# Kernel optimization log

Measured on AMD Instinct MI355X. Metric: run time of the kernel, lower is better.

The kernel has to match this reference:

```python
import jax, jax.numpy as jnp
import numpy as np

B, C, N = 8, 256, 4096

def setup_inputs() -> dict:
    key = jax.random.key(0)
    k1, k2, k3 = jax.random.split(key, 3)
    pts_feat = jax.random.normal(k1, (B, C, N), dtype=jnp.float32)
    # Conv1d(channels, channels, 1, bias=False) weight is [C_out, C_in, 1] -> store as [C_out, C_in]
    scale = 1.0 / np.sqrt(C)
    Wq = jax.random.uniform(k2, (C, C), dtype=jnp.float32, minval=-scale, maxval=scale)
    Wk = jax.random.uniform(k3, (C, C), dtype=jnp.float32, minval=-scale, maxval=scale)
    return {"pts_feat": pts_feat, "Wq": Wq, "Wk": Wk}

def reference(pts_feat, Wq, Wk):
    # 1x1 conv == channel-wise matmul. x_q: [B, N, C], x_k: [B, C, N]
    x_q = jnp.einsum('bcn,dc->bnd', pts_feat, Wq)
    x_k = jnp.einsum('bcn,dc->bdn', pts_feat, Wk)
    logits = jnp.einsum('bnc,bcm->bnm', x_q, x_k)          # [B, N, N]
    attn = jax.nn.softmax(logits, axis=-1)
    attn = attn / (1e-8 + attn.sum(axis=-1, keepdims=True))
    # torch.einsum('bnn,bnc->bnc', attn, feat) takes the DIAGONAL of attn
    # and scales each point's raw feature vector by it (no contraction).
    diag = jnp.diagonal(attn, axis1=1, axis2=2)            # [B, N]
    x_attn = pts_feat * diag[:, None, :]                   # [B, C, N]
    return x_attn
```

## Files before the change

kernel.cpp:

```cpp
#include <hip/hip_runtime.h>
#include <hip/hip_bf16.h>
#include <cstdint>

#define B_ 8
#define C_ 256
#define N_ 4096

typedef __bf16 bf16;
typedef __bf16 bf16x8 __attribute__((ext_vector_type(8)));
typedef float f32x4 __attribute__((ext_vector_type(4)));
typedef unsigned int u32;

__device__ __forceinline__ void async_ld16(const void* g, void* l) {
  __builtin_amdgcn_global_load_lds(
      (const __attribute__((address_space(1))) void*)g,
      (__attribute__((address_space(3))) void*)l, 16, 0, 0);
}

__device__ __forceinline__ float bh2f(unsigned short u) {
  union { u32 i; float f; } x; x.i = ((u32)u) << 16; return x.f;
}
__device__ __forceinline__ unsigned short f2bh(float f) {
  union { float f; u32 i; } x; x.f = f;
  u32 i = x.i + 0x7fffu + ((x.i >> 16) & 1u);
  return (unsigned short)(i >> 16);
}

__device__ __forceinline__ bool wave_sniff_fp32(const unsigned short* p) {
  int l = threadIdx.x & 63;
  unsigned short u = p[2 * l];
  int e = (u >> 7) & 0xff;
  unsigned long long m = __ballot(e >= 112 && e <= 142);
  return __popcll(m) < 32;
}

__global__ __launch_bounds__(256) void k_pre(const void* __restrict__ Wqv,
                                             const void* __restrict__ Wkv,
                                             const void* __restrict__ Fv,
                                             unsigned short* __restrict__ Mt,
                                             unsigned short* __restrict__ Ft) {
  __shared__ float wkcol[C_];
  __shared__ unsigned short tile[64 * 66];
  int bid = blockIdx.x;
  int t = threadIdx.x;
  if (bid < 256) {
    bool fq = wave_sniff_fp32((const unsigned short*)Wqv);
    bool fk = wave_sniff_fp32((const unsigned short*)Wkv);
    int d = bid, c = t;
    if (fk)
      wkcol[c] = ((const float*)Wkv)[c * C_ + d];
    else
      wkcol[c] = bh2f(((const unsigned short*)Wkv)[c * C_ + d]);
    __syncthreads();
    float acc = 0.f;
    if (fq) {
      for (int e0 = 0; e0 < C_; e0 += 16) {
        float wq[16];
#pragma unroll
        for (int j = 0; j < 16; ++j) wq[j] = ((const float*)Wqv)[(e0 + j) * C_ + c];
#pragma unroll
        for (int j = 0; j < 16; ++j) acc += wkcol[e0 + j] * wq[j];
      }
    } else {
      for (int e0 = 0; e0 < C_; e0 += 16) {
        float wq[16];
#pragma unroll
        for (int j = 0; j < 16; ++j) wq[j] = bh2f(((const unsigned short*)Wqv)[(e0 + j) * C_ + c]);
#pragma unroll
        for (int j = 0; j < 16; ++j) acc += wkcol[e0 + j] * wq[j];
      }
    }
    Mt[(size_t)d * C_ + c] = f2bh(acc * 1.44269504f);
    return;
  }
  bool f32 = wave_sniff_fp32((const unsigned short*)Fv);
  int id = bid - 256;
  int n0 = (id & 63) * 64, c0 = ((id >> 6) & 3) * 64, b = id >> 8;
#pragma unroll
  for (int p = 0; p < 2; ++p) {
    int c = (t >> 3) + 32 * p;
    int n = (t & 7) * 8;
    size_t off = (size_t)(b * C_ + c0 + c) * N_ + n0 + n;
    unsigned short vals[8];
    if (f32) {
      const float* src = (const float*)Fv + off;
      float4 v0 = *(const float4*)(src);
      float4 v1 = *(const float4*)(src + 4);
      vals[0] = f2bh(v0.x); vals[1] = f2bh(v0.y); vals[2] = f2bh(v0.z); vals[3] = f2bh(v0.w);
      vals[4] = f2bh(v1.x); vals[5] = f2bh(v1.y); vals[6] = f2bh(v1.z); vals[7] = f2bh(v1.w);
    } else {
      uint4 v = *(const uint4*)((const unsigned short*)Fv + off);
      vals[0] = (unsigned short)(v.x & 0xffffu); vals[1] = (unsigned short)(v.x >> 16);
      vals[2] = (unsigned short)(v.y & 0xffffu); vals[3] = (unsigned short)(v.y >> 16);
      vals[4] = (unsigned short)(v.z & 0xffffu); vals[5] = (unsigned short)(v.z >> 16);
      vals[6] = (unsigned short)(v.w & 0xffffu); vals[7] = (unsigned short)(v.w >> 16);
    }
#pragma unroll
    for (int s = 0; s < 8; ++s) tile[c * 66 + n + s] = vals[s];
  }
  __syncthreads();
#pragma unroll
  for (int p = 0; p < 2; ++p) {
    int n = (t >> 3) + 32 * p;
    int c8 = (t & 7) * 8;
    u32 o[4];
#pragma unroll
    for (int k = 0; k < 4; ++k) {
      unsigned short lo = tile[(c8 + 2 * k) * 66 + n];
      unsigned short hi = tile[(c8 + 2 * k + 1) * 66 + n];
      o[k] = ((u32)hi << 16) | lo;
    }
    uint4 ov; ov.x = o[0]; ov.y = o[1]; ov.z = o[2]; ov.w = o[3];
    *(uint4*)(Ft + ((size_t)(b * N_ + n0 + n) * C_ + c0 + c8)) = ov;
  }
}

__global__ __launch_bounds__(256, 4) void k_proj(const bf16* __restrict__ Ft,
                                                 const bf16* __restrict__ Mt,
                                                 bf16* __restrict__ G) {
  __shared__ bf16 As[8 * 64 * 32];
  int n0 = blockIdx.x * 64;
  int b = blockIdx.y;
  int d0 = blockIdx.z * 128;
  int t = threadIdx.x, w = t >> 6, l = t & 63;
  int lr = l & 15, lq = l >> 4;
  int wn = w * 32;
  const size_t fbase = (size_t)b * N_ * C_;

  int srow = t >> 2;
  int schunk = ((t & 3) ^ ((t >> 3) & 3)) * 8;
#pragma unroll
  for (int kc = 0; kc < 8; ++kc)
    async_ld16(Ft + fbase + (size_t)(n0 + srow) * C_ + kc * 32 + schunk,
               As + kc * 2048 + t * 8);

  bf16x8 bb[2][8];
#pragma unroll
  for (int j = 0; j < 2; ++j)
#pragma unroll
    for (int kc = 0; kc < 8; ++kc)
      bb[j][kc] = *(const bf16x8*)(Mt + (size_t)(d0 + wn + 16 * j + lr) * C_ + kc * 32 + lq * 8);

  __syncthreads();
  int rchunk = (lq ^ ((lr >> 1) & 3)) * 8;
  f32x4 acc[4][2] = {};
#pragma unroll
  for (int kc = 0; kc < 8; ++kc) {
#pragma unroll
    for (int i = 0; i < 4; ++i) {
      bf16x8 a = *(const bf16x8*)(As + kc * 2048 + (16 * i + lr) * 32 + rchunk);
#pragma unroll
      for (int j = 0; j < 2; ++j)
        acc[i][j] = __builtin_amdgcn_mfma_f32_16x16x32_bf16(a, bb[j][kc], acc[i][j], 0, 0, 0);
    }
  }
  __syncthreads();
  unsigned short* Cs = (unsigned short*)As;
#pragma unroll
  for (int i = 0; i < 4; ++i)
#pragma unroll
    for (int j = 0; j < 2; ++j)
#pragma unroll
      for (int r = 0; r < 4; ++r)
        Cs[(16 * i + lq * 4 + r) * 136 + wn + 16 * j + lr] = f2bh(acc[i][j][r]);
  __syncthreads();
#pragma unroll
  for (int p = 0; p < 4; ++p) {
    int idx = p * 256 + t;
    int row = idx >> 4, c8 = idx & 15;
    uint4 v = *(const uint4*)(Cs + row * 136 + c8 * 8);
    *(uint4*)(G + fbase + (size_t)(n0 + row) * C_ + d0 + c8 * 8) = v;
  }
}

__global__ __launch_bounds__(256, 4) void k_attn(const bf16* __restrict__ G,
                                                 const bf16* __restrict__ Ft,
                                                 float* __restrict__ snn,
                                                 float* __restrict__ lsum) {
  __shared__ bf16 Ks[2][32 * 256];
  int bid = blockIdx.x;
  int b = bid & 7, q = (bid >> 3) & 3, ntile = bid >> 5;
  int n0 = ntile * 128;
  int t = threadIdx.x, w = t >> 6, l = t & 63;
  int lr = l & 15, lq = l >> 4;
  int wrow = w * 32;
  const size_t gbase = (size_t)b * N_ * C_;

  bf16x8 a[2][8];
#pragma unroll
  for (int i = 0; i < 2; ++i)
#pragma unroll
    for (int kc = 0; kc < 8; ++kc)
      a[i][kc] = *(const bf16x8*)(G + gbase + (size_t)(n0 + wrow + 16 * i + lr) * C_ + kc * 32 + lq * 8);

  float part[8];
#pragma unroll
  for (int s = 0; s < 8; ++s) part[s] = 0.f;

  int m_base = q * 1024;
  bool has_diag = (q == (ntile >> 3));
  int dbase = (ntile & 7) * 4;

  int soff[4];
#pragma unroll
  for (int p = 0; p < 4; ++p) {
    int flat = p * 256 + t;
    int kc = flat >> 7;
    int r = (flat >> 2) & 31;
    int col8 = flat & 3;
    soff[p] = r * C_ + kc * 32 + ((col8 ^ ((r >> 1) & 3)) * 8);
  }
  int rchunk = (lq ^ ((lr >> 1) & 3)) * 8;

#pragma unroll
  for (int p = 0; p < 4; ++p)
    async_ld16(Ft + gbase + (size_t)m_base * C_ + soff[p],
               (bf16*)Ks + (p * 256 + t) * 8);
  asm volatile("s_waitcnt vmcnt(0)" ::: "memory");
  __builtin_amdgcn_s_barrier();

  for (int it = 0; it < 32; ++it) {
    int cur = it & 1;
    if (it < 31) {
      int m0 = m_base + (it + 1) * 32;
#pragma unroll
      for (int p = 0; p < 4; ++p)
        async_ld16(Ft + gbase + (size_t)m0 * C_ + soff[p],
                   (bf16*)Ks + (cur ^ 1) * 8192 + (p * 256 + t) * 8);
    }
    const bf16* ks = (const bf16*)Ks + cur * 8192;
    f32x4 acc[2][2] = {};
#pragma unroll
    for (int kc = 0; kc < 8; ++kc) {
      bf16x8 b0 = *(const bf16x8*)(ks + kc * 1024 + lr * 32 + rchunk);
      bf16x8 b1 = *(const bf16x8*)(ks + kc * 1024 + (16 + lr) * 32 + rchunk);
      acc[0][0] = __builtin_amdgcn_mfma_f32_16x16x32_bf16(a[0][kc], b0, acc[0][0], 0, 0, 0);
      acc[1][0] = __builtin_amdgcn_mfma_f32_16x16x32_bf16(a[1][kc], b0, acc[1][0], 0, 0, 0);
      acc[0][1] = __builtin_amdgcn_mfma_f32_16x16x32_bf16(a[0][kc], b1, acc[0][1], 0, 0, 0);
      acc[1][1] = __builtin_amdgcn_mfma_f32_16x16x32_bf16(a[1][kc], b1, acc[1][1], 0, 0, 0);
    }
    bool dit = has_diag && ((it >> 2) == (ntile & 7));
#pragma unroll
    for (int i = 0; i < 2; ++i)
#pragma unroll
      for (int j = 0; j < 2; ++j)
#pragma unroll
        for (int r = 0; r < 4; ++r) {
          float e = __builtin_amdgcn_exp2f(acc[i][j][r]);
          part[i * 4 + r] += e;
          if (dit) {
            int rloc = wrow + 16 * i + lq * 4 + r;
            int cloc = 16 * j + lr;
            if ((it - dbase) * 32 + cloc == rloc) snn[b * N_ + n0 + rloc] = e;
          }
        }
    if (it < 31) {
      asm volatile("s_waitcnt vmcnt(0)" ::: "memory");
      __builtin_amdgcn_s_barrier();
    }
  }

#pragma unroll
  for (int s = 0; s < 8; ++s) {
    float v = part[s];
    v += __shfl_xor(v, 1);
    v += __shfl_xor(v, 2);
    v += __shfl_xor(v, 4);
    v += __shfl_xor(v, 8);
    part[s] = v;
  }
  if (lr == 0) {
#pragma unroll
    for (int i = 0; i < 2; ++i)
#pragma unroll
      for (int r = 0; r < 4; ++r)
        lsum[((size_t)q * B_ + b) * N_ + n0 + wrow + 16 * i + lq * 4 + r] = part[i * 4 + r];
  }
}

__global__ __launch_bounds__(256) void k_scale(const void* __restrict__ Fv,
                                               const float* __restrict__ snn,
                                               const float* __restrict__ lsum,
                                               void* __restrict__ Outv) {
  __shared__ __align__(16) float dd_lds[64];
  bool f32 = wave_sniff_fp32((const unsigned short*)Fv);
  int bid = blockIdx.x;
  int b = bid >> 6, n0 = (bid & 63) * 64;
  int t = threadIdx.x;
  if (t < 64) {
    int n = n0 + t;
    float s = snn[(size_t)b * N_ + n];
    float ls = 0.f;
#pragma unroll
    for (int p = 0; p < 4; ++p) ls += lsum[((size_t)p * B_ + b) * N_ + n];
    dd_lds[t] = s / (ls * (1.0f + 1e-8f));
  }
  __syncthreads();
  const size_t fb = (size_t)b * C_ * N_;
  if (f32) {
    const float* F = (const float*)Fv;
    float* O = (float*)Outv;
#pragma unroll
    for (int p = 0; p < 16; ++p) {
      int idx = p * 256 + t;
      int c = idx >> 4, ch = idx & 15;
      size_t off = fb + (size_t)c * N_ + n0 + ch * 4;
      float4 v = *(const float4*)(F + off);
      float4 d = *(const float4*)(&dd_lds[ch * 4]);
      float4 o;
      o.x = v.x * d.x; o.y = v.y * d.y; o.z = v.z * d.z; o.w = v.w * d.w;
      *(float4*)(O + off) = o;
    }
  } else {
    const unsigned short* F = (const unsigned short*)Fv;
    unsigned short* O = (unsigned short*)Outv;
#pragma unroll
    for (int p = 0; p < 8; ++p) {
      int idx = p * 256 + t;
      int c = idx >> 3, ch = idx & 7;
      size_t off = fb + (size_t)c * N_ + n0 + ch * 8;
      uint4 v = *(const uint4*)(F + off);
      u32 vv[4] = {v.x, v.y, v.z, v.w};
      u32 o[4];
#pragma unroll
      for (int k = 0; k < 4; ++k) {
        float lo = bh2f((unsigned short)(vv[k] & 0xffffu)) * dd_lds[ch * 8 + 2 * k];
        float hi = bh2f((unsigned short)(vv[k] >> 16)) * dd_lds[ch * 8 + 2 * k + 1];
        o[k] = ((u32)f2bh(hi) << 16) | f2bh(lo);
      }
      uint4 ov; ov.x = o[0]; ov.y = o[1]; ov.z = o[2]; ov.w = o[3];
      *(uint4*)(O + off) = ov;
    }
  }
}

extern "C" void kernel_launch(void* const* d_in, const int* in_sizes, int n_in,
                              void* d_out, int out_size, void* d_ws, size_t ws_size,
                              hipStream_t stream) {
  (void)in_sizes; (void)n_in; (void)out_size; (void)ws_size;
  const void* F = d_in[0];
  const void* Wq = d_in[1];
  const void* Wk = d_in[2];
  char* ws = (char*)d_ws;
  bf16* Ft = (bf16*)(ws);
  bf16* G = (bf16*)(ws + (16u << 20));
  char* tail = ws + (32u << 20);
  float* snn = (float*)(tail);
  float* lsum = (float*)(tail + 131072);
  bf16* Mt = (bf16*)(tail + 131072 + 524288);

  k_pre<<<256 + 2048, 256, 0, stream>>>(Wq, Wk, F, (unsigned short*)Mt, (unsigned short*)Ft);
  k_proj<<<dim3(N_ / 64, B_, 2), 256, 0, stream>>>(Ft, Mt, G);
  k_attn<<<1024, 256, 0, stream>>>(G, Ft, snn, lsum);
  k_scale<<<512, 256, 0, stream>>>(F, snn, lsum, d_out);
}
```

Measured before the change: 169.8 us.

## Enlarge attention tiles to 512 rows with a 4-stage async K pipeline

The attention kernel now uses 512-thread blocks covering 512 query rows, with each wave holding 64 rows (four 16-row A fragments). This raises reuse of each K tile loaded into LDS and cuts the grid from 1024 blocks to 256. The double buffer becomes a 4-slot ring with three tiles in flight, paced by partial vmcnt waits so there is one barrier per iteration instead of a full drain, and s_setprio is raised around the MFMA loop. The trade-off is higher register use from 32 A fragments and 8 accumulators, plus fewer blocks, which could leave CUs idle or lower occupancy.

```diff
diff --git a/kernel.cpp b/kernel.cpp
--- a/kernel.cpp
+++ b/kernel.cpp
@@ -173,38 +173,38 @@
   }
 }
 
-__global__ __launch_bounds__(256, 4) void k_attn(const bf16* __restrict__ G,
-                                                 const bf16* __restrict__ Ft,
-                                                 float* __restrict__ snn,
-                                                 float* __restrict__ lsum) {
-  __shared__ bf16 Ks[2][32 * 256];
+__global__ __launch_bounds__(512) void k_attn(const bf16* __restrict__ G,
+                                              const bf16* __restrict__ Ft,
+                                              float* __restrict__ snn,
+                                              float* __restrict__ lsum) {
+  __shared__ bf16 Ks[4][32 * 256];
   int bid = blockIdx.x;
   int b = bid & 7, q = (bid >> 3) & 3, ntile = bid >> 5;
-  int n0 = ntile * 128;
+  int n0 = ntile * 512;
   int t = threadIdx.x, w = t >> 6, l = t & 63;
   int lr = l & 15, lq = l >> 4;
-  int wrow = w * 32;
+  int wrow = w * 64;
   const size_t gbase = (size_t)b * N_ * C_;
 
-  bf16x8 a[2][8];
-#pragma unroll
-  for (int i = 0; i < 2; ++i)
+  bf16x8 a[32];
+#pragma unroll
+  for (int i = 0; i < 4; ++i)
 #pragma unroll
     for (int kc = 0; kc < 8; ++kc)
-      a[i][kc] = *(const bf16x8*)(G + gbase + (size_t)(n0 + wrow + 16 * i + lr) * C_ + kc * 32 + lq * 8);
-
-  float part[8];
-#pragma unroll
-  for (int s = 0; s < 8; ++s) part[s] = 0.f;
+      a[i * 8 + kc] = *(const bf16x8*)(G + gbase + (size_t)(n0 + wrow + 16 * i + lr) * C_ + kc * 32 + lq * 8);
+
+  float part[16];
+#pragma unroll
+  for (int s = 0; s < 16; ++s) part[s] = 0.f;
 
   int m_base = q * 1024;
-  bool has_diag = (q == (ntile >> 3));
-  int dbase = (ntile & 7) * 4;
-
-  int soff[4];
-#pragma unroll
-  for (int p = 0; p < 4; ++p) {
-    int flat = p * 256 + t;
+  bool has_diag = (q == (ntile >> 1));
+  int dbase = (ntile & 1) * 16;
+
+  int soff[2];
+#pragma unroll
+  for (int p = 0; p < 2; ++p) {
+    int flat = p * 512 + t;
     int kc = flat >> 7;
     int r = (flat >> 2) & 31;
     int col8 = flat & 3;
@@ -213,55 +213,61 @@
   int rchunk = (lq ^ ((lr >> 1) & 3)) * 8;
 
 #pragma unroll
-  for (int p = 0; p < 4; ++p)
-    async_ld16(Ft + gbase + (size_t)m_base * C_ + soff[p],
-               (bf16*)Ks + (p * 256 + t) * 8);
-  asm volatile("s_waitcnt vmcnt(0)" ::: "memory");
-  __builtin_amdgcn_s_barrier();
+  for (int s = 0; s < 3; ++s)
+#pragma unroll
+    for (int p = 0; p < 2; ++p)
+      async_ld16(Ft + gbase + (size_t)(m_base + s * 32) * C_ + soff[p],
+                 (bf16*)Ks + s * 8192 + (p * 512 + t) * 8);
 
   for (int it = 0; it < 32; ++it) {
-    int cur = it & 1;
-    if (it < 31) {
-      int m0 = m_base + (it + 1) * 32;
-#pragma unroll
-      for (int p = 0; p < 4; ++p)
-        async_ld16(Ft + gbase + (size_t)m0 * C_ + soff[p],
-                   (bf16*)Ks + (cur ^ 1) * 8192 + (p * 256 + t) * 8);
-    }
-    const bf16* ks = (const bf16*)Ks + cur * 8192;
-    f32x4 acc[2][2] = {};
+    if (it <= 29) {
+      asm volatile("s_waitcnt vmcnt(4)" ::: "memory");
+    } else if (it == 30) {
+      asm volatile("s_waitcnt vmcnt(2)" ::: "memory");
+    } else {
+      asm volatile("s_waitcnt vmcnt(0)" ::: "memory");
+    }
+    __builtin_amdgcn_s_barrier();
+    if (it <= 28) {
+      int m0 = m_base + (it + 3) * 32;
+      bf16* dst = (bf16*)Ks + ((it + 3) & 3) * 8192;
+#pragma unroll
+      for (int p = 0; p < 2; ++p)
+        async_ld16(Ft + gbase + (size_t)m0 * C_ + soff[p], dst + (p * 512 + t) * 8);
+    }
+
+    const bf16* ks = (const bf16*)Ks + (it & 3) * 8192;
+    f32x4 acc[8] = {};
+    __builtin_amdgcn_s_setprio(1);
 #pragma unroll
     for (int kc = 0; kc < 8; ++kc) {
       bf16x8 b0 = *(const bf16x8*)(ks + kc * 1024 + lr * 32 + rchunk);
       bf16x8 b1 = *(const bf16x8*)(ks + kc * 1024 + (16 + lr) * 32 + rchunk);
-      acc[0][0] = __builtin_amdgcn_mfma_f32_16x16x32_bf16(a[0][kc], b0, acc[0][0], 0, 0, 0);
-      acc[1][0] = __builtin_amdgcn_mfma_f32_16x16x32_bf16(a[1][kc], b0, acc[1][0], 0, 0, 0);
-      acc[0][1] = __builtin_amdgcn_mfma_f32_16x16x32_bf16(a[0][kc], b1, acc[0][1], 0, 0, 0);
-      acc[1][1] = __builtin_amdgcn_mfma_f32_16x16x32_bf16(a[1][kc], b1, acc[1][1], 0, 0, 0);
-    }
-    bool dit = has_diag && ((it >> 2) == (ntile & 7));
-#pragma unroll
-    for (int i = 0; i < 2; ++i)
+#pragma unroll
+      for (int i = 0; i < 4; ++i) {
+        acc[i * 2 + 0] = __builtin_amdgcn_mfma_f32_16x16x32_bf16(a[i * 8 + kc], b0, acc[i * 2 + 0], 0, 0, 0);
+        acc[i * 2 + 1] = __builtin_amdgcn_mfma_f32_16x16x32_bf16(a[i * 8 + kc], b1, acc[i * 2 + 1], 0, 0, 0);
+      }
+    }
+    __builtin_amdgcn_s_setprio(0);
+
+#pragma unroll
+    for (int i = 0; i < 4; ++i) {
+      bool dit = has_diag && (it == dbase + 2 * w + (i >> 1));
 #pragma unroll
       for (int j = 0; j < 2; ++j)
 #pragma unroll
         for (int r = 0; r < 4; ++r) {
-          float e = __builtin_amdgcn_exp2f(acc[i][j][r]);
+          float e = __builtin_amdgcn_exp2f(acc[i * 2 + j][r]);
           part[i * 4 + r] += e;
-          if (dit) {
-            int rloc = wrow + 16 * i + lq * 4 + r;
-            int cloc = 16 * j + lr;
-            if ((it - dbase) * 32 + cloc == rloc) snn[b * N_ + n0 + rloc] = e;
-          }
+          if (dit && j == (i & 1) && lr == lq * 4 + r)
+            snn[b * N_ + n0 + wrow + 16 * i + lq * 4 + r] = e;
         }
-    if (it < 31) {
-      asm volatile("s_waitcnt vmcnt(0)" ::: "memory");
-      __builtin_amdgcn_s_barrier();
-    }
-  }
-
-#pragma unroll
-  for (int s = 0; s < 8; ++s) {
+    }
+  }
+
+#pragma unroll
+  for (int s = 0; s < 16; ++s) {
     float v = part[s];
     v += __shfl_xor(v, 1);
     v += __shfl_xor(v, 2);
@@ -271,7 +277,7 @@
   }
   if (lr == 0) {
 #pragma unroll
-    for (int i = 0; i < 2; ++i)
+    for (int i = 0; i < 4; ++i)
 #pragma unroll
       for (int r = 0; r < 4; ++r)
         lsum[((size_t)q * B_ + b) * N_ + n0 + wrow + 16 * i + lq * 4 + r] = part[i * 4 + r];
@@ -351,6 +357,6 @@
 
   k_pre<<<256 + 2048, 256, 0, stream>>>(Wq, Wk, F, (unsigned short*)Mt, (unsigned short*)Ft);
   k_proj<<<dim3(N_ / 64, B_, 2), 256, 0, stream>>>(Ft, Mt, G);
-  k_attn<<<1024, 256, 0, stream>>>(G, Ft, snn, lsum);
+  k_attn<<<256, 512, 0, stream>>>(G, Ft, snn, lsum);
   k_scale<<<512, 256, 0, stream>>>(F, snn, lsum, d_out);
 }
```

Result: no change. 171.3 us (+0.9%).

## Fuse feature transpose into projection kernel, keeping tile in LDS

Applied to the files above, without the earlier changes.

The transpose/bf16 conversion of the features is moved out of the precompute kernel into the projection kernel. Each block now transposes a full 64-point by 256-channel slab, writes Ft to global memory, and also writes the swizzled tile straight into LDS for the MFMA projection. Both output halves of G are computed in-block instead of split across grid.z, so Ft is no longer re-read from global memory and one launch boundary goes away. In exchange there are fewer, larger blocks (512 instead of 1024), more LDS per block, and serialized transpose and compute phases within each block.

```diff
diff --git a/kernel.cpp b/kernel.cpp
--- a/kernel.cpp
+++ b/kernel.cpp
@@ -34,142 +34,138 @@
   return __popcll(m) < 32;
 }
 
-__global__ __launch_bounds__(256) void k_pre(const void* __restrict__ Wqv,
-                                             const void* __restrict__ Wkv,
-                                             const void* __restrict__ Fv,
-                                             unsigned short* __restrict__ Mt,
-                                             unsigned short* __restrict__ Ft) {
+__global__ __launch_bounds__(256) void k_mt(const void* __restrict__ Wqv,
+                                            const void* __restrict__ Wkv,
+                                            unsigned short* __restrict__ Mt) {
   __shared__ float wkcol[C_];
-  __shared__ unsigned short tile[64 * 66];
-  int bid = blockIdx.x;
   int t = threadIdx.x;
-  if (bid < 256) {
-    bool fq = wave_sniff_fp32((const unsigned short*)Wqv);
-    bool fk = wave_sniff_fp32((const unsigned short*)Wkv);
-    int d = bid, c = t;
-    if (fk)
-      wkcol[c] = ((const float*)Wkv)[c * C_ + d];
-    else
-      wkcol[c] = bh2f(((const unsigned short*)Wkv)[c * C_ + d]);
-    __syncthreads();
-    float acc = 0.f;
-    if (fq) {
-      for (int e0 = 0; e0 < C_; e0 += 16) {
-        float wq[16];
-#pragma unroll
-        for (int j = 0; j < 16; ++j) wq[j] = ((const float*)Wqv)[(e0 + j) * C_ + c];
-#pragma unroll
-        for (int j = 0; j < 16; ++j) acc += wkcol[e0 + j] * wq[j];
-      }
-    } else {
-      for (int e0 = 0; e0 < C_; e0 += 16) {
-        float wq[16];
-#pragma unroll
-        for (int j = 0; j < 16; ++j) wq[j] = bh2f(((const unsigned short*)Wqv)[(e0 + j) * C_ + c]);
-#pragma unroll
-        for (int j = 0; j < 16; ++j) acc += wkcol[e0 + j] * wq[j];
-      }
-    }
-    Mt[(size_t)d * C_ + c] = f2bh(acc * 1.44269504f);
-    return;
-  }
-  bool f32 = wave_sniff_fp32((const unsigned short*)Fv);
-  int id = bid - 256;
-  int n0 = (id & 63) * 64, c0 = ((id >> 6) & 3) * 64, b = id >> 8;
-#pragma unroll
-  for (int p = 0; p < 2; ++p) {
-    int c = (t >> 3) + 32 * p;
-    int n = (t & 7) * 8;
-    size_t off = (size_t)(b * C_ + c0 + c) * N_ + n0 + n;
-    unsigned short vals[8];
-    if (f32) {
-      const float* src = (const float*)Fv + off;
-      float4 v0 = *(const float4*)(src);
-      float4 v1 = *(const float4*)(src + 4);
-      vals[0] = f2bh(v0.x); vals[1] = f2bh(v0.y); vals[2] = f2bh(v0.z); vals[3] = f2bh(v0.w);
-      vals[4] = f2bh(v1.x); vals[5] = f2bh(v1.y); vals[6] = f2bh(v1.z); vals[7] = f2bh(v1.w);
-    } else {
-      uint4 v = *(const uint4*)((const unsigned short*)Fv + off);
-      vals[0] = (unsigned short)(v.x & 0xffffu); vals[1] = (unsigned short)(v.x >> 16);
-      vals[2] = (unsigned short)(v.y & 0xffffu); vals[3] = (unsigned short)(v.y >> 16);
-      vals[4] = (unsigned short)(v.z & 0xffffu); vals[5] = (unsigned short)(v.z >> 16);
-      vals[6] = (unsigned short)(v.w & 0xffffu); vals[7] = (unsigned short)(v.w >> 16);
-    }
-#pragma unroll
-    for (int s = 0; s < 8; ++s) tile[c * 66 + n + s] = vals[s];
-  }
+  bool fq = wave_sniff_fp32((const unsigned short*)Wqv);
+  bool fk = wave_sniff_fp32((const unsigned short*)Wkv);
+  int d = blockIdx.x, c = t;
+  if (fk)
+    wkcol[c] = ((const float*)Wkv)[c * C_ + d];
+  else
+    wkcol[c] = bh2f(((const unsigned short*)Wkv)[c * C_ + d]);
   __syncthreads();
-#pragma unroll
-  for (int p = 0; p < 2; ++p) {
-    int n = (t >> 3) + 32 * p;
-    int c8 = (t & 7) * 8;
-    u32 o[4];
-#pragma unroll
-    for (int k = 0; k < 4; ++k) {
-      unsigned short lo = tile[(c8 + 2 * k) * 66 + n];
-      unsigned short hi = tile[(c8 + 2 * k + 1) * 66 + n];
-      o[k] = ((u32)hi << 16) | lo;
-    }
-    uint4 ov; ov.x = o[0]; ov.y = o[1]; ov.z = o[2]; ov.w = o[3];
-    *(uint4*)(Ft + ((size_t)(b * N_ + n0 + n) * C_ + c0 + c8)) = ov;
-  }
-}
-
-__global__ __launch_bounds__(256, 4) void k_proj(const bf16* __restrict__ Ft,
-                                                 const bf16* __restrict__ Mt,
-                                                 bf16* __restrict__ G) {
+  float acc = 0.f;
+  if (fq) {
+    for (int e0 = 0; e0 < C_; e0 += 16) {
+      float wq[16];
+#pragma unroll
+      for (int j = 0; j < 16; ++j) wq[j] = ((const float*)Wqv)[(e0 + j) * C_ + c];
+#pragma unroll
+      for (int j = 0; j < 16; ++j) acc += wkcol[e0 + j] * wq[j];
+    }
+  } else {
+    for (int e0 = 0; e0 < C_; e0 += 16) {
+      float wq[16];
+#pragma unroll
+      for (int j = 0; j < 16; ++j) wq[j] = bh2f(((const unsigned short*)Wqv)[(e0 + j) * C_ + c]);
+#pragma unroll
+      for (int j = 0; j < 16; ++j) acc += wkcol[e0 + j] * wq[j];
+    }
+  }
+  Mt[(size_t)d * C_ + c] = f2bh(acc * 1.44269504f);
+}
+
+__global__ __launch_bounds__(256, 2) void k_tp(const void* __restrict__ Fv,
+                                               const bf16* __restrict__ Mt,
+                                               unsigned short* __restrict__ Ft,
+                                               bf16* __restrict__ G) {
+  __shared__ unsigned short tile[128 * 70];
   __shared__ bf16 As[8 * 64 * 32];
   int n0 = blockIdx.x * 64;
   int b = blockIdx.y;
-  int d0 = blockIdx.z * 128;
-  int t = threadIdx.x, w = t >> 6, l = t & 63;
-  int lr = l & 15, lq = l >> 4;
+  int t = threadIdx.x;
+  bool f32 = wave_sniff_fp32((const unsigned short*)Fv);
+
+#pragma unroll
+  for (int hp = 0; hp < 2; ++hp) {
+    if (hp) __syncthreads();
+#pragma unroll
+    for (int p = 0; p < 4; ++p) {
+      int cl = (t >> 3) + 32 * p;
+      int n = (t & 7) * 8;
+      size_t off = (size_t)(b * C_ + hp * 128 + cl) * N_ + n0 + n;
+      unsigned short vals[8];
+      if (f32) {
+        const float* src = (const float*)Fv + off;
+        float4 v0 = *(const float4*)(src);
+        float4 v1 = *(const float4*)(src + 4);
+        vals[0] = f2bh(v0.x); vals[1] = f2bh(v0.y); vals[2] = f2bh(v0.z); vals[3] = f2bh(v0.w);
+        vals[4] = f2bh(v1.x); vals[5] = f2bh(v1.y); vals[6] = f2bh(v1.z); vals[7] = f2bh(v1.w);
+      } else {
+        uint4 v = *(const uint4*)((const unsigned short*)Fv + off);
+        vals[0] = (unsigned short)(v.x & 0xffffu); vals[1] = (unsigned short)(v.x >> 16);
+        vals[2] = (unsigned short)(v.y & 0xffffu); vals[3] = (unsigned short)(v.y >> 16);
+        vals[4] = (unsigned short)(v.z & 0xffffu); vals[5] = (unsigned short)(v.z >> 16);
+        vals[6] = (unsigned short)(v.w & 0xffffu); vals[7] = (unsigned short)(v.w >> 16);
+      }
+#pragma unroll
+      for (int s = 0; s < 8; ++s) tile[cl * 70 + n + s] = vals[s];
+    }
+    __syncthreads();
+#pragma unroll
+    for (int p = 0; p < 4; ++p) {
+      int idx = p * 256 + t;
+      int n = idx >> 4, oc = idx & 15;
+      u32 o[4];
+#pragma unroll
+      for (int k = 0; k < 4; ++k) {
+        unsigned short lo = tile[(oc * 8 + 2 * k) * 70 + n];
+        unsigned short hi = tile[(oc * 8 + 2 * k + 1) * 70 + n];
+        o[k] = ((u32)hi << 16) | lo;
+      }
+      uint4 ov; ov.x = o[0]; ov.y = o[1]; ov.z = o[2]; ov.w = o[3];
+      *(uint4*)(Ft + ((size_t)(b * N_ + n0 + n)) * C_ + hp * 128 + oc * 8) = ov;
+      int gc = hp * 16 + oc;
+      int kc = gc >> 2, col8 = gc & 3;
+      *(uint4*)((unsigned short*)As + kc * 2048 + n * 32 + (col8 ^ ((n >> 1) & 3)) * 8) = ov;
+    }
+  }
+  __syncthreads();
+
+  int w = t >> 6, l = t & 63, lr = l & 15, lq = l >> 4;
   int wn = w * 32;
+  int rchunk = (lq ^ ((lr >> 1) & 3)) * 8;
   const size_t fbase = (size_t)b * N_ * C_;
-
-  int srow = t >> 2;
-  int schunk = ((t & 3) ^ ((t >> 3) & 3)) * 8;
-#pragma unroll
-  for (int kc = 0; kc < 8; ++kc)
-    async_ld16(Ft + fbase + (size_t)(n0 + srow) * C_ + kc * 32 + schunk,
-               As + kc * 2048 + t * 8);
-
-  bf16x8 bb[2][8];
-#pragma unroll
-  for (int j = 0; j < 2; ++j)
-#pragma unroll
-    for (int kc = 0; kc < 8; ++kc)
-      bb[j][kc] = *(const bf16x8*)(Mt + (size_t)(d0 + wn + 16 * j + lr) * C_ + kc * 32 + lq * 8);
-
-  __syncthreads();
-  int rchunk = (lq ^ ((lr >> 1) & 3)) * 8;
-  f32x4 acc[4][2] = {};
-#pragma unroll
-  for (int kc = 0; kc < 8; ++kc) {
-#pragma unroll
-    for (int i = 0; i < 4; ++i) {
-      bf16x8 a = *(const bf16x8*)(As + kc * 2048 + (16 * i + lr) * 32 + rchunk);
+#pragma unroll
+  for (int jp = 0; jp < 2; ++jp) {
+    int d0 = jp * 128;
+    bf16x8 bb[2][8];
+#pragma unroll
+    for (int j = 0; j < 2; ++j)
+#pragma unroll
+      for (int kc = 0; kc < 8; ++kc)
+        bb[j][kc] = *(const bf16x8*)(Mt + (size_t)(d0 + wn + 16 * j + lr) * C_ + kc * 32 + lq * 8);
+    f32x4 acc[4][2] = {};
+#pragma unroll
+    for (int kc = 0; kc < 8; ++kc) {
+#pragma unroll
+      for (int i = 0; i < 4; ++i) {
+        bf16x8 a = *(const bf16x8*)(As + kc * 2048 + (16 * i + lr) * 32 + rchunk);
+#pragma unroll
+        for (int j = 0; j < 2; ++j)
+          acc[i][j] = __builtin_amdgcn_mfma_f32_16x16x32_bf16(a, bb[j][kc], acc[i][j], 0, 0, 0);
+      }
+    }
+    __syncthreads();
+    unsigned short* Cs = (unsigned short*)tile;
+#pragma unroll
+    for (int i = 0; i < 4; ++i)
 #pragma unroll
       for (int j = 0; j < 2; ++j)
-        acc[i][j] = __builtin_amdgcn_mfma_f32_16x16x32_bf16(a, bb[j][kc], acc[i][j], 0, 0, 0);
-    }
-  }
-  __syncthreads();
-  unsigned short* Cs = (unsigned short*)As;
-#pragma unroll
-  for (int i = 0; i < 4; ++i)
-#pragma unroll
-    for (int j = 0; j < 2; ++j)
-#pragma unroll
-      for (int r = 0; r < 4; ++r)
-        Cs[(16 * i + lq * 4 + r) * 136 + wn + 16 * j + lr] = f2bh(acc[i][j][r]);
-  __syncthreads();
-#pragma unroll
-  for (int p = 0; p < 4; ++p) {
-    int idx = p * 256 + t;
-    int row = idx >> 4, c8 = idx & 15;
-    uint4 v = *(const uint4*)(Cs + row * 136 + c8 * 8);
-    *(uint4*)(G + fbase + (size_t)(n0 + row) * C_ + d0 + c8 * 8) = v;
+#pragma unroll
+        for (int r = 0; r < 4; ++r)
+          Cs[(16 * i + lq * 4 + r) * 136 + wn + 16 * j + lr] = f2bh(acc[i][j][r]);
+    __syncthreads();
+#pragma unroll
+    for (int p = 0; p < 4; ++p) {
+      int idx = p * 256 + t;
+      int row = idx >> 4, c8 = idx & 15;
+      uint4 v = *(const uint4*)(Cs + row * 136 + c8 * 8);
+      *(uint4*)(G + fbase + (size_t)(n0 + row) * C_ + d0 + c8 * 8) = v;
+    }
   }
 }
 
@@ -349,8 +345,8 @@
   float* lsum = (float*)(tail + 131072);
   bf16* Mt = (bf16*)(tail + 131072 + 524288);
 
-  k_pre<<<256 + 2048, 256, 0, stream>>>(Wq, Wk, F, (unsigned short*)Mt, (unsigned short*)Ft);
-  k_proj<<<dim3(N_ / 64, B_, 2), 256, 0, stream>>>(Ft, Mt, G);
+  k_mt<<<256, 256, 0, stream>>>(Wq, Wk, (unsigned short*)Mt);
+  k_tp<<<dim3(N_ / 64, B_), 256, 0, stream>>>(F, Mt, (unsigned short*)Ft, G);
   k_attn<<<1024, 256, 0, stream>>>(G, Ft, snn, lsum);
   k_scale<<<512, 256, 0, stream>>>(F, snn, lsum, d_out);
 }
```

Result: no change. 169.9 us (+0.1%).
